# Performance work log

Hardware: AMD Instinct MI355X
Metric: run time of the kernel (lower is better)

The kernel has to match this reference:

```python
import jax, jax.numpy as jnp
import numpy as np

# Module config (matches init_kwargs)
IN_CH, K, N_LAYERS, STRIDE = 4, 4, 2, 2
N_QUBITS = 6           # ceil(log2(4*4*4)) = 6
DIM = 2 ** N_QUBITS    # 64 amplitudes
B, H = 128, 128


def setup_inputs() -> dict:
    key = jax.random.key(0)
    k1, k2 = jax.random.split(key)
    x = jax.random.normal(k1, (B, IN_CH, H, H), dtype=jnp.float32)
    weights = jax.random.normal(k2, (N_LAYERS, N_QUBITS, 3), dtype=jnp.float32)
    return {"x": x, "weights": weights}


def _rot(phi, theta, omega):
    # PennyLane Rot(phi, theta, omega) = RZ(omega) RY(theta) RZ(phi)
    c = jnp.cos(theta / 2).astype(jnp.complex64)
    s = jnp.sin(theta / 2).astype(jnp.complex64)
    ep = jnp.exp(-0.5j * (phi + omega).astype(jnp.complex64))
    em = jnp.exp(-0.5j * (phi - omega).astype(jnp.complex64))
    row0 = jnp.stack([ep * c, -jnp.conj(em) * s])
    row1 = jnp.stack([em * s, jnp.conj(ep) * c])
    return jnp.stack([row0, row1])  # (2,2) complex64


def _apply_1q(state, U, w):
    # state: (N, 2,...,2); wire w -> axis 1+w (wire 0 most significant)
    s = jnp.moveaxis(state, 1 + w, -1)
    s = s @ U.T
    return jnp.moveaxis(s, -1, 1 + w)


def _apply_cnot(state, c, t):
    s = jnp.moveaxis(state, (1 + c, 1 + t), (1, 2))
    s = jnp.stack([s[:, 0], s[:, 1, ::-1]], axis=1)
    return jnp.moveaxis(s, (1, 2), (1 + c, 1 + t))


def _circuit(feat, weights):
    # feat: (N, DIM) amplitude-embedded & normalized features
    state = feat.astype(jnp.complex64).reshape((-1,) + (2,) * N_QUBITS)
    ranges = [(l % (N_QUBITS - 1)) + 1 for l in range(N_LAYERS)]
    for _rep in range(N_LAYERS):  # circuit applies the full template n_layers times
        for l in range(N_LAYERS):
            for w in range(N_QUBITS):
                U = _rot(weights[l, w, 0], weights[l, w, 1], weights[l, w, 2])
                state = _apply_1q(state, U, w)
            r = ranges[l]
            for w in range(N_QUBITS):
                state = _apply_cnot(state, w, (w + r) % N_QUBITS)
    probs = state.real ** 2 + state.imag ** 2
    z = []
    for w in range(N_QUBITS):
        p = jnp.moveaxis(probs, 1 + w, 1).reshape(probs.shape[0], 2, -1)
        z.append(p[:, 0].sum(-1) - p[:, 1].sum(-1))  # <Z_w>
    return jnp.stack(z, axis=1)  # (N, n_qubits)


def reference(x, weights):
    Bx, C, Hx, Wx = x.shape
    oh = (Hx - K) // STRIDE + 1
    idx = (jnp.arange(oh) * STRIDE)[:, None] + jnp.arange(K)  # (oh, K)
    p = x[:, :, idx, :]       # (B, C, oh, K, W)
    p = p[..., idx]           # (B, C, oh, K, oh, K)
    p = jnp.transpose(p, (0, 2, 4, 1, 3, 5)).reshape(Bx * oh * oh, C * K * K)
    feat = jnp.pad(p, ((0, 0), (0, DIM - C * K * K)))  # AmplitudeEmbedding pad_with=0
    feat = feat / jnp.linalg.norm(feat, axis=1, keepdims=True)  # normalize=True
    z = _circuit(feat, weights)                        # (B*oh*oh, n_qubits)
    out = z.reshape(Bx, oh, oh, N_QUBITS).transpose(0, 3, 1, 2)
    return out  # (B, n_qubits, oh, oh)
```

## Files before the change

kernel.cpp:

```cpp
#include <hip/hip_runtime.h>

#define NQ     6
#define DIM    64
#define OH     63
#define HH     128
#define CIN    4
#define NB     128
#define FSTR   72

typedef __attribute__((ext_vector_type(8))) short  short8;
typedef __attribute__((ext_vector_type(4))) float  f32x4;

__device__ __forceinline__ unsigned bf16_rne(float f) {
    unsigned u = __builtin_bit_cast(unsigned, f);
    return (u + 0x7fffu + ((u >> 16) & 1u)) >> 16;
}

__global__ __launch_bounds__(64) void build_u(const float* __restrict__ wts,
                                              float2* __restrict__ Ut) {
    const int i   = threadIdx.x;
    const int col = blockIdx.x;
    float2 amp = make_float2(i == col ? 1.0f : 0.0f, 0.0f);
    const int ranges[2] = {1, 2};

    for (int rep = 0; rep < 2; ++rep) {
        for (int l = 0; l < 2; ++l) {
            for (int w = 0; w < NQ; ++w) {
                const float phi = wts[(l * NQ + w) * 3 + 0];
                const float th  = wts[(l * NQ + w) * 3 + 1];
                const float om  = wts[(l * NQ + w) * 3 + 2];
                const float hc = cosf(0.5f * th);
                const float hs = sinf(0.5f * th);
                const float ap = -0.5f * (phi + om);
                const float am = -0.5f * (phi - om);
                const float2 ep = make_float2(cosf(ap), sinf(ap));
                const float2 em = make_float2(cosf(am), sinf(am));
                const float2 U00 = make_float2( ep.x * hc,  ep.y * hc);
                const float2 U01 = make_float2(-em.x * hs,  em.y * hs);
                const float2 U10 = make_float2( em.x * hs,  em.y * hs);
                const float2 U11 = make_float2( ep.x * hc, -ep.y * hc);
                const int p = 5 - w;
                const int bbit = (i >> p) & 1;
                const float px = __shfl_xor(amp.x, 1 << p, 64);
                const float py = __shfl_xor(amp.y, 1 << p, 64);
                const float2 ua = bbit ? U11 : U00;
                const float2 ub = bbit ? U10 : U01;
                float2 na;
                na.x = ua.x * amp.x - ua.y * amp.y + ub.x * px - ub.y * py;
                na.y = ua.x * amp.y + ua.y * amp.x + ub.x * py + ub.y * px;
                amp = na;
            }
            const int r = ranges[l];
            for (int w = 0; w < NQ; ++w) {
                const int pc = 5 - w;
                const int pt = 5 - ((w + r) % NQ);
                const int src = i ^ (((i >> pc) & 1) << pt);
                const float nx = __shfl(amp.x, src, 64);
                const float ny = __shfl(amp.y, src, 64);
                amp = make_float2(nx, ny);
            }
        }
    }
    Ut[col * DIM + i] = amp;
}

__global__ __launch_bounds__(64) void wprep(const float2* __restrict__ Ut,
                                            short* __restrict__ wfrag) {
    const int f = blockIdx.x;
    const int l = threadIdx.x;
    const int lo = f >> 4;
    const int mt = (f & 15) >> 1;
    const int t  = f & 1;
    const int m  = mt * 16 + (l & 15);
    short8 v;
#pragma unroll
    for (int j = 0; j < 8; ++j) {
        const int k = t * 32 + (l >> 4) * 8 + j;
        const float2 u = Ut[k * DIM + (m & 63)];
        const float val = (m < 64) ? u.x : u.y;
        const unsigned h = bf16_rne(val);
        if (lo == 0) {
            v[j] = (short)h;
        } else {
            const float fh = __builtin_bit_cast(float, h << 16);
            v[j] = (short)bf16_rne(val - fh);
        }
    }
    ((int4*)wfrag)[f * 64 + l] = __builtin_bit_cast(int4, v);
}

__global__ __launch_bounds__(256, 2) void qconv_mfma(const float* __restrict__ x,
                                                     const short* __restrict__ wfrag,
                                                     float* __restrict__ out) {
    __shared__ __align__(16) short sF[4][16 * FSTR];
    __shared__ __align__(16) short sP[4][16 * FSTR];

    const int tid  = threadIdx.x;
    const int lane = tid & 63;
    const int wv   = tid >> 6;
    const int n    = lane & 15;
    const int qq   = lane >> 4;

    const int row = blockIdx.x * 4 + wv;
    const int b   = row / OH;
    const int oy  = row - b * OH;

    short8 whi[8][2], wlo[8][2];
    {
        const int4* wp = (const int4*)wfrag;
#pragma unroll
        for (int mt = 0; mt < 8; ++mt)
#pragma unroll
            for (int t = 0; t < 2; ++t) {
                const int f = mt * 2 + t;
                whi[mt][t] = __builtin_bit_cast(short8, wp[f * 64 + lane]);
                wlo[mt][t] = __builtin_bit_cast(short8, wp[(16 + f) * 64 + lane]);
            }
    }

    short8 sfr[2];
#pragma unroll
    for (int t = 0; t < 2; ++t) {
        short8 v;
#pragma unroll
        for (int j = 0; j < 8; ++j) {
            const int i = t * 32 + qq * 8 + j;
            unsigned short s;
            if (n < 6)       s = ((i >> (5 - n)) & 1) ? 0xBF80 : 0x3F80;
            else if (n == 6) s = 0x3F80;
            else             s = 0;
            v[j] = (short)s;
        }
        sfr[t] = v;
    }

    short* myF = sF[wv];
    short* myP = sP[wv];

    const float* xb = x + (size_t)b * CIN * HH * HH;
    const float* bptr[8];
#pragma unroll
    for (int it = 0; it < 8; ++it) {
        const int kp  = it * 4 + qq;
        const int c   = kp >> 3;
        const int kh  = (kp >> 1) & 3;
        const int kwh = kp & 1;
        bptr[it] = xb + (c * HH + 2 * oy + kh) * HH + 2 * kwh;
    }

    float2 fv[8];
#pragma unroll
    for (int it = 0; it < 8; ++it) fv[it] = *(const float2*)(bptr[it] + 2 * n);

    for (int ch = 0; ch < 4; ++ch) {
#pragma unroll
        for (int it = 0; it < 8; ++it) {
            const unsigned lo = bf16_rne(fv[it].x);
            const unsigned hi = bf16_rne(fv[it].y);
            ((unsigned*)myF)[n * (FSTR / 2) + it * 4 + qq] = lo | (hi << 16);
        }
        {
            const int oxe = min(ch * 16 + 16 + n, OH - 1);
#pragma unroll
            for (int it = 0; it < 8; ++it)
                fv[it] = *(const float2*)(bptr[it] + 2 * oxe);
        }

        const short8 b0 = *(const short8*)(myF + n * FSTR + qq * 8);
        const short8 b1 = *(const short8*)(myF + n * FSTR + 32 + qq * 8);

        f32x4 acc[8];
#pragma unroll
        for (int mt = 0; mt < 8; ++mt) acc[mt] = (f32x4){0.f, 0.f, 0.f, 0.f};
#pragma unroll
        for (int mt = 0; mt < 8; ++mt) {
            acc[mt] = __builtin_amdgcn_mfma_f32_16x16x32_bf16(whi[mt][0], b0, acc[mt], 0, 0, 0);
            acc[mt] = __builtin_amdgcn_mfma_f32_16x16x32_bf16(whi[mt][1], b1, acc[mt], 0, 0, 0);
            acc[mt] = __builtin_amdgcn_mfma_f32_16x16x32_bf16(wlo[mt][0], b0, acc[mt], 0, 0, 0);
            acc[mt] = __builtin_amdgcn_mfma_f32_16x16x32_bf16(wlo[mt][1], b1, acc[mt], 0, 0, 0);
        }

#pragma unroll
        for (int mt = 0; mt < 4; ++mt) {
            const float p0 = acc[mt][0] * acc[mt][0] + acc[mt + 4][0] * acc[mt + 4][0];
            const float p1 = acc[mt][1] * acc[mt][1] + acc[mt + 4][1] * acc[mt + 4][1];
            const float p2 = acc[mt][2] * acc[mt][2] + acc[mt + 4][2] * acc[mt + 4][2];
            const float p3 = acc[mt][3] * acc[mt][3] + acc[mt + 4][3] * acc[mt + 4][3];
            const unsigned w0 = (__builtin_bit_cast(unsigned, p0) >> 16) |
                                (__builtin_bit_cast(unsigned, p1) & 0xFFFF0000u);
            const unsigned w1 = (__builtin_bit_cast(unsigned, p2) >> 16) |
                                (__builtin_bit_cast(unsigned, p3) & 0xFFFF0000u);
            *((uint2*)(((unsigned*)myP) + n * (FSTR / 2) + mt * 8 + qq * 2)) =
                make_uint2(w0, w1);
        }

        const short8 p0f = *(const short8*)(myP + n * FSTR + qq * 8);
        const short8 p1f = *(const short8*)(myP + n * FSTR + 32 + qq * 8);
        f32x4 c2 = (f32x4){0.f, 0.f, 0.f, 0.f};
        c2 = __builtin_amdgcn_mfma_f32_16x16x32_bf16(sfr[0], p0f, c2, 0, 0, 0);
        c2 = __builtin_amdgcn_mfma_f32_16x16x32_bf16(sfr[1], p1f, c2, 0, 0, 0);

        const float norm = __shfl(c2[2], 16 + n, 64);
        const float inv  = 1.0f / norm;
        const int ox = ch * 16 + n;
        if (ox < OH) {
            float* ob = out + ((size_t)b * NQ * OH + oy) * OH + ox;
            if (qq == 0) {
#pragma unroll
                for (int r = 0; r < 4; ++r) ob[(size_t)r * (OH * OH)] = c2[r] * inv;
            } else if (qq == 1) {
                ob[(size_t)4 * (OH * OH)] = c2[0] * inv;
                ob[(size_t)5 * (OH * OH)] = c2[1] * inv;
            }
        }
    }
}

extern "C" void kernel_launch(void* const* d_in, const int* in_sizes, int n_in,
                              void* d_out, int out_size, void* d_ws, size_t ws_size,
                              hipStream_t stream) {
    const float* x   = (const float*)d_in[0];
    const float* wts = (const float*)d_in[1];
    float* out = (float*)d_out;

    float2* Ut    = (float2*)d_ws;
    short*  wfrag = (short*)((char*)d_ws + 64 * 1024);

    build_u<<<64, 64, 0, stream>>>(wts, Ut);
    wprep<<<32, 64, 0, stream>>>(Ut, wfrag);
    qconv_mfma<<<(NB * OH) / 4, 256, 0, stream>>>(x, wfrag, out);
}
```

Before: 114.2 us.

## Merge prep kernels and load patches directly into MFMA B fragments

Combines build_u and wprep into a single one-block prep kernel. It computes the rotation matrices once in shared memory and keeps the unitary in LDS, which removes one launch and a global round trip. The main kernel now reorders the K dimension so each lane gathers its eight contiguous patch elements directly from global memory into registers. This drops the sF shared-memory staging and the software-pipelined prefetch. It also uses packed bf16 conversion instructions where available, at the cost of losing prefetch overlap for the global loads.

```diff
diff --git a/kernel.cpp b/kernel.cpp
--- a/kernel.cpp
+++ b/kernel.cpp
@@ -1,99 +1,127 @@
 #include <hip/hip_runtime.h>
 
-#define NQ     6
-#define DIM    64
-#define OH     63
-#define HH     128
-#define CIN    4
-#define NB     128
-#define FSTR   72
-
-typedef __attribute__((ext_vector_type(8))) short  short8;
-typedef __attribute__((ext_vector_type(4))) float  f32x4;
-
-__device__ __forceinline__ unsigned bf16_rne(float f) {
+#define NQ   6
+#define DIM  64
+#define OH   63
+#define HH   128
+#define CIN  4
+#define NB   128
+#define PSTR 80
+
+typedef __attribute__((ext_vector_type(8))) short short8;
+typedef __attribute__((ext_vector_type(4))) float f32x4;
+
+__device__ __forceinline__ unsigned bf16_rne_u(float f) {
     unsigned u = __builtin_bit_cast(unsigned, f);
     return (u + 0x7fffu + ((u >> 16) & 1u)) >> 16;
 }
 
-__global__ __launch_bounds__(64) void build_u(const float* __restrict__ wts,
-                                              float2* __restrict__ Ut) {
-    const int i   = threadIdx.x;
-    const int col = blockIdx.x;
-    float2 amp = make_float2(i == col ? 1.0f : 0.0f, 0.0f);
-    const int ranges[2] = {1, 2};
-
-    for (int rep = 0; rep < 2; ++rep) {
-        for (int l = 0; l < 2; ++l) {
-            for (int w = 0; w < NQ; ++w) {
-                const float phi = wts[(l * NQ + w) * 3 + 0];
-                const float th  = wts[(l * NQ + w) * 3 + 1];
-                const float om  = wts[(l * NQ + w) * 3 + 2];
-                const float hc = cosf(0.5f * th);
-                const float hs = sinf(0.5f * th);
-                const float ap = -0.5f * (phi + om);
-                const float am = -0.5f * (phi - om);
-                const float2 ep = make_float2(cosf(ap), sinf(ap));
-                const float2 em = make_float2(cosf(am), sinf(am));
-                const float2 U00 = make_float2( ep.x * hc,  ep.y * hc);
-                const float2 U01 = make_float2(-em.x * hs,  em.y * hs);
-                const float2 U10 = make_float2( em.x * hs,  em.y * hs);
-                const float2 U11 = make_float2( ep.x * hc, -ep.y * hc);
-                const int p = 5 - w;
-                const int bbit = (i >> p) & 1;
-                const float px = __shfl_xor(amp.x, 1 << p, 64);
-                const float py = __shfl_xor(amp.y, 1 << p, 64);
-                const float2 ua = bbit ? U11 : U00;
-                const float2 ub = bbit ? U10 : U01;
-                float2 na;
-                na.x = ua.x * amp.x - ua.y * amp.y + ub.x * px - ub.y * py;
-                na.y = ua.x * amp.y + ua.y * amp.x + ub.x * py + ub.y * px;
-                amp = na;
+#if __has_builtin(__builtin_amdgcn_cvt_pk_bf16_f32)
+__device__ __forceinline__ unsigned pk_bf16(float a, float b) {
+    typedef __attribute__((ext_vector_type(2))) __bf16 bf16x2_t;
+    bf16x2_t v = __builtin_amdgcn_cvt_pk_bf16_f32(a, b);
+    return __builtin_bit_cast(unsigned, v);
+}
+#else
+__device__ __forceinline__ unsigned pk_bf16(float a, float b) {
+    return bf16_rne_u(a) | (bf16_rne_u(b) << 16);
+}
+#endif
+
+__global__ __launch_bounds__(1024) void prep(const float* __restrict__ wts,
+                                             short* __restrict__ wfrag) {
+    __shared__ float2 rotm[12][4];
+    __shared__ float2 sUt[DIM * DIM];
+
+    const int tid = threadIdx.x;
+
+    if (tid < 12) {
+        const float phi = wts[tid * 3 + 0];
+        const float th  = wts[tid * 3 + 1];
+        const float om  = wts[tid * 3 + 2];
+        const float hc = cosf(0.5f * th);
+        const float hs = sinf(0.5f * th);
+        const float ap = -0.5f * (phi + om);
+        const float am = -0.5f * (phi - om);
+        const float2 ep = make_float2(cosf(ap), sinf(ap));
+        const float2 em = make_float2(cosf(am), sinf(am));
+        rotm[tid][0] = make_float2( ep.x * hc,  ep.y * hc);
+        rotm[tid][1] = make_float2(-em.x * hs,  em.y * hs);
+        rotm[tid][2] = make_float2( em.x * hs,  em.y * hs);
+        rotm[tid][3] = make_float2( ep.x * hc, -ep.y * hc);
+    }
+    __syncthreads();
+
+    const int lane = tid & 63;
+    const int wv   = tid >> 6;
+
+#pragma unroll
+    for (int cc = 0; cc < 4; ++cc) {
+        const int col = wv * 4 + cc;
+        float2 amp = make_float2(lane == col ? 1.0f : 0.0f, 0.0f);
+#pragma unroll
+        for (int rep = 0; rep < 2; ++rep) {
+#pragma unroll
+            for (int l = 0; l < 2; ++l) {
+#pragma unroll
+                for (int w = 0; w < NQ; ++w) {
+                    const float2 U00 = rotm[l * 6 + w][0];
+                    const float2 U01 = rotm[l * 6 + w][1];
+                    const float2 U10 = rotm[l * 6 + w][2];
+                    const float2 U11 = rotm[l * 6 + w][3];
+                    const int p = 5 - w;
+                    const int bbit = (lane >> p) & 1;
+                    const float px = __shfl_xor(amp.x, 1 << p, 64);
+                    const float py = __shfl_xor(amp.y, 1 << p, 64);
+                    const float2 ua = bbit ? U11 : U00;
+                    const float2 ub = bbit ? U10 : U01;
+                    float2 na;
+                    na.x = ua.x * amp.x - ua.y * amp.y + ub.x * px - ub.y * py;
+                    na.y = ua.x * amp.y + ua.y * amp.x + ub.x * py + ub.y * px;
+                    amp = na;
+                }
+                const int r = (l == 0) ? 1 : 2;
+#pragma unroll
+                for (int w = 0; w < NQ; ++w) {
+                    const int pc = 5 - w;
+                    const int pt = 5 - ((w + r) % NQ);
+                    const int src = lane ^ (((lane >> pc) & 1) << pt);
+                    const float nx = __shfl(amp.x, src, 64);
+                    const float ny = __shfl(amp.y, src, 64);
+                    amp = make_float2(nx, ny);
+                }
             }
-            const int r = ranges[l];
-            for (int w = 0; w < NQ; ++w) {
-                const int pc = 5 - w;
-                const int pt = 5 - ((w + r) % NQ);
-                const int src = i ^ (((i >> pc) & 1) << pt);
-                const float nx = __shfl(amp.x, src, 64);
-                const float ny = __shfl(amp.y, src, 64);
-                amp = make_float2(nx, ny);
-            }
-        }
-    }
-    Ut[col * DIM + i] = amp;
-}
-
-__global__ __launch_bounds__(64) void wprep(const float2* __restrict__ Ut,
-                                            short* __restrict__ wfrag) {
-    const int f = blockIdx.x;
-    const int l = threadIdx.x;
-    const int lo = f >> 4;
-    const int mt = (f & 15) >> 1;
-    const int t  = f & 1;
-    const int m  = mt * 16 + (l & 15);
-    short8 v;
-#pragma unroll
-    for (int j = 0; j < 8; ++j) {
-        const int k = t * 32 + (l >> 4) * 8 + j;
-        const float2 u = Ut[k * DIM + (m & 63)];
-        const float val = (m < 64) ? u.x : u.y;
-        const unsigned h = bf16_rne(val);
-        if (lo == 0) {
-            v[j] = (short)h;
-        } else {
+        }
+        sUt[col * DIM + lane] = amp;
+    }
+    __syncthreads();
+
+    {
+        const int f  = tid >> 6;
+        const int l  = lane;
+        const int mt = f >> 1;
+        const int t  = f & 1;
+        const int m  = mt * 16 + (l & 15);
+        short8 vhi, vlo;
+#pragma unroll
+        for (int j = 0; j < 8; ++j) {
+            const int k = t * 32 + (l >> 4) * 8 + j;
+            const float2 u = sUt[k * DIM + (m & 63)];
+            const float val = (m < 64) ? u.x : u.y;
+            const unsigned h = bf16_rne_u(val);
+            vhi[j] = (short)h;
             const float fh = __builtin_bit_cast(float, h << 16);
-            v[j] = (short)bf16_rne(val - fh);
-        }
-    }
-    ((int4*)wfrag)[f * 64 + l] = __builtin_bit_cast(int4, v);
+            vlo[j] = (short)bf16_rne_u(val - fh);
+        }
+        ((int4*)wfrag)[f * 64 + l]        = __builtin_bit_cast(int4, vhi);
+        ((int4*)wfrag)[(16 + f) * 64 + l] = __builtin_bit_cast(int4, vlo);
+    }
 }
 
 __global__ __launch_bounds__(256, 2) void qconv_mfma(const float* __restrict__ x,
                                                      const short* __restrict__ wfrag,
                                                      float* __restrict__ out) {
-    __shared__ __align__(16) short sF[4][16 * FSTR];
-    __shared__ __align__(16) short sP[4][16 * FSTR];
+    __shared__ __align__(16) short sP[4][16 * PSTR];
 
     const int tid  = threadIdx.x;
     const int lane = tid & 63;
@@ -134,50 +162,48 @@
         sfr[t] = v;
     }
 
-    short* myF = sF[wv];
+    const int c0  = qq >> 1;
+    const int kh0 = (qq & 1) * 2;
+    const float* xb  = x + (size_t)b * CIN * HH * HH;
+    const float* r00 = xb + ((c0    ) * HH + 2 * oy + kh0    ) * HH;
+    const float* r01 = xb + ((c0    ) * HH + 2 * oy + kh0 + 1) * HH;
+    const float* r10 = xb + ((c0 + 2) * HH + 2 * oy + kh0    ) * HH;
+    const float* r11 = xb + ((c0 + 2) * HH + 2 * oy + kh0 + 1) * HH;
+
     short* myP = sP[wv];
 
-    const float* xb = x + (size_t)b * CIN * HH * HH;
-    const float* bptr[8];
-#pragma unroll
-    for (int it = 0; it < 8; ++it) {
-        const int kp  = it * 4 + qq;
-        const int c   = kp >> 3;
-        const int kh  = (kp >> 1) & 3;
-        const int kwh = kp & 1;
-        bptr[it] = xb + (c * HH + 2 * oy + kh) * HH + 2 * kwh;
-    }
-
-    float2 fv[8];
-#pragma unroll
-    for (int it = 0; it < 8; ++it) fv[it] = *(const float2*)(bptr[it] + 2 * n);
-
+#pragma unroll
     for (int ch = 0; ch < 4; ++ch) {
-#pragma unroll
-        for (int it = 0; it < 8; ++it) {
-            const unsigned lo = bf16_rne(fv[it].x);
-            const unsigned hi = bf16_rne(fv[it].y);
-            ((unsigned*)myF)[n * (FSTR / 2) + it * 4 + qq] = lo | (hi << 16);
-        }
-        {
-            const int oxe = min(ch * 16 + 16 + n, OH - 1);
-#pragma unroll
-            for (int it = 0; it < 8; ++it)
-                fv[it] = *(const float2*)(bptr[it] + 2 * oxe);
-        }
-
-        const short8 b0 = *(const short8*)(myF + n * FSTR + qq * 8);
-        const short8 b1 = *(const short8*)(myF + n * FSTR + 32 + qq * 8);
+        const int ox  = ch * 16 + n;
+        const int oxl = min(ox, OH - 1);
+        const int fo  = 2 * oxl;
+
+        const float2 a0 = *(const float2*)(r00 + fo);
+        const float2 a1 = *(const float2*)(r00 + fo + 2);
+        const float2 b0 = *(const float2*)(r01 + fo);
+        const float2 b1 = *(const float2*)(r01 + fo + 2);
+        const float2 e0 = *(const float2*)(r10 + fo);
+        const float2 e1 = *(const float2*)(r10 + fo + 2);
+        const float2 d0 = *(const float2*)(r11 + fo);
+        const float2 d1 = *(const float2*)(r11 + fo + 2);
+
+        uint4 u0, u1;
+        u0.x = pk_bf16(a0.x, a0.y);  u0.y = pk_bf16(a1.x, a1.y);
+        u0.z = pk_bf16(b0.x, b0.y);  u0.w = pk_bf16(b1.x, b1.y);
+        u1.x = pk_bf16(e0.x, e0.y);  u1.y = pk_bf16(e1.x, e1.y);
+        u1.z = pk_bf16(d0.x, d0.y);  u1.w = pk_bf16(d1.x, d1.y);
+        const short8 bf0 = __builtin_bit_cast(short8, u0);
+        const short8 bf1 = __builtin_bit_cast(short8, u1);
 
         f32x4 acc[8];
 #pragma unroll
         for (int mt = 0; mt < 8; ++mt) acc[mt] = (f32x4){0.f, 0.f, 0.f, 0.f};
 #pragma unroll
         for (int mt = 0; mt < 8; ++mt) {
-            acc[mt] = __builtin_amdgcn_mfma_f32_16x16x32_bf16(whi[mt][0], b0, acc[mt], 0, 0, 0);
-            acc[mt] = __builtin_amdgcn_mfma_f32_16x16x32_bf16(whi[mt][1], b1, acc[mt], 0, 0, 0);
-            acc[mt] = __builtin_amdgcn_mfma_f32_16x16x32_bf16(wlo[mt][0], b0, acc[mt], 0, 0, 0);
-            acc[mt] = __builtin_amdgcn_mfma_f32_16x16x32_bf16(wlo[mt][1], b1, acc[mt], 0, 0, 0);
+            acc[mt] = __builtin_amdgcn_mfma_f32_16x16x32_bf16(whi[mt][0], bf0, acc[mt], 0, 0, 0);
+            acc[mt] = __builtin_amdgcn_mfma_f32_16x16x32_bf16(whi[mt][1], bf1, acc[mt], 0, 0, 0);
+            acc[mt] = __builtin_amdgcn_mfma_f32_16x16x32_bf16(wlo[mt][0], bf0, acc[mt], 0, 0, 0);
+            acc[mt] = __builtin_amdgcn_mfma_f32_16x16x32_bf16(wlo[mt][1], bf1, acc[mt], 0, 0, 0);
         }
 
 #pragma unroll
@@ -186,23 +212,20 @@
             const float p1 = acc[mt][1] * acc[mt][1] + acc[mt + 4][1] * acc[mt + 4][1];
             const float p2 = acc[mt][2] * acc[mt][2] + acc[mt + 4][2] * acc[mt + 4][2];
             const float p3 = acc[mt][3] * acc[mt][3] + acc[mt + 4][3] * acc[mt + 4][3];
-            const unsigned w0 = (__builtin_bit_cast(unsigned, p0) >> 16) |
-                                (__builtin_bit_cast(unsigned, p1) & 0xFFFF0000u);
-            const unsigned w1 = (__builtin_bit_cast(unsigned, p2) >> 16) |
-                                (__builtin_bit_cast(unsigned, p3) & 0xFFFF0000u);
-            *((uint2*)(((unsigned*)myP) + n * (FSTR / 2) + mt * 8 + qq * 2)) =
+            const unsigned w0 = pk_bf16(p0, p1);
+            const unsigned w1 = pk_bf16(p2, p3);
+            *((uint2*)(((unsigned*)myP) + n * (PSTR / 2) + mt * 8 + qq * 2)) =
                 make_uint2(w0, w1);
         }
 
-        const short8 p0f = *(const short8*)(myP + n * FSTR + qq * 8);
-        const short8 p1f = *(const short8*)(myP + n * FSTR + 32 + qq * 8);
+        const short8 p0f = *(const short8*)(myP + n * PSTR + qq * 8);
+        const short8 p1f = *(const short8*)(myP + n * PSTR + 32 + qq * 8);
         f32x4 c2 = (f32x4){0.f, 0.f, 0.f, 0.f};
         c2 = __builtin_amdgcn_mfma_f32_16x16x32_bf16(sfr[0], p0f, c2, 0, 0, 0);
         c2 = __builtin_amdgcn_mfma_f32_16x16x32_bf16(sfr[1], p1f, c2, 0, 0, 0);
 
         const float norm = __shfl(c2[2], 16 + n, 64);
         const float inv  = 1.0f / norm;
-        const int ox = ch * 16 + n;
         if (ox < OH) {
             float* ob = out + ((size_t)b * NQ * OH + oy) * OH + ox;
             if (qq == 0) {
@@ -222,11 +245,8 @@
     const float* x   = (const float*)d_in[0];
     const float* wts = (const float*)d_in[1];
     float* out = (float*)d_out;
-
-    float2* Ut    = (float2*)d_ws;
-    short*  wfrag = (short*)((char*)d_ws + 64 * 1024);
-
-    build_u<<<64, 64, 0, stream>>>(wts, Ut);
-    wprep<<<32, 64, 0, stream>>>(Ut, wfrag);
+    short* wfrag = (short*)d_ws;
+
+    prep<<<1, 1024, 0, stream>>>(wts, wfrag);
     qconv_mfma<<<(NB * OH) / 4, 256, 0, stream>>>(x, wfrag, out);
 }
```

After: 137.6 us. 1.2x slower.
